# Kernel tuning notes

Measured on AMD Instinct MI355X. Metric: run time of the kernel, lower is better.

## Reference

```python
import jax, jax.numpy as jnp
import numpy as np

N = 12288
F_IN = 128
F_OUT = 128


def setup_inputs() -> dict:
    key = jax.random.key(0)
    k1, k2, k3, k4, k5, k6, k7 = jax.random.split(key, 7)
    stdv = 1.0 / np.sqrt(F_OUT)
    return {
        "feats": jax.random.normal(k1, (N, F_IN), dtype=jnp.float32),
        "node_adj": jax.random.normal(k2, (N, N), dtype=jnp.float32),
        "edge_adj": jax.random.normal(k3, (N, N), dtype=jnp.float32),
        # params: msg_type='concat' -> node_weight is [2*in, out]
        "node_weight": jax.random.uniform(k4, (2 * F_IN, F_OUT), dtype=jnp.float32, minval=-stdv, maxval=stdv),
        "node_bias": jax.random.uniform(k5, (F_OUT,), dtype=jnp.float32, minval=-stdv, maxval=stdv),
        "edge_weight": jax.random.uniform(k6, (F_IN, F_OUT), dtype=jnp.float32, minval=-stdv, maxval=stdv),
        "edge_bias": jax.random.uniform(k7, (F_OUT,), dtype=jnp.float32, minval=-stdv, maxval=stdv),
    }


def reference(feats, node_adj, edge_adj, node_weight, node_bias, edge_weight, edge_bias):
    # msg_type == 'concat': two masked spmms over signed adjacency, concat along features
    pos = (node_adj > 0).astype(feats.dtype)  # [N, N]
    neg = (node_adj < 0).astype(feats.dtype)  # [N, N]
    node_support = jnp.concatenate([pos @ feats, neg @ feats], axis=1)  # [N, 2*F_IN]
    node_output = node_support @ node_weight + node_bias  # [N, F_OUT]
    edge_support = edge_adj @ feats  # [N, F_IN]
    edge_output = edge_support @ edge_weight + edge_bias  # [N, F_OUT]
    return jax.nn.relu(node_output) + edge_output
```

## Files before the change

kernel.cpp:

```cpp
#include <hip/hip_runtime.h>
#include <stdint.h>

#define N_ROWS 12288
#define GSZ (128 * 12288)
#define NPART_OFF (9437184 / 4)
#define EPART_OFF ((9437184 + 6291456) / 4)

typedef __attribute__((ext_vector_type(8))) short bf16x8;
typedef __attribute__((ext_vector_type(4))) float f32x4;

__device__ __forceinline__ uint32_t f2bf(float x) {
  union { float f; uint32_t u; } c; c.f = x;
  return (c.u + 0x7FFFu + ((c.u >> 16) & 1u)) >> 16;
}
__device__ __forceinline__ uint32_t pk_bf(float a, float b) {
  return f2bf(a) | (f2bf(b) << 16);
}
__device__ __forceinline__ uint32_t pk_pos(float a, float b) {
  return (a > 0.f ? 0x3F80u : 0u) | (b > 0.f ? 0x3F800000u : 0u);
}
__device__ __forceinline__ uint32_t pk_neg(float a, float b) {
  return (a < 0.f ? 0x3F80u : 0u) | (b < 0.f ? 0x3F800000u : 0u);
}

__global__ __launch_bounds__(256) void gw_kernel(
    const float* __restrict__ feats, const float* __restrict__ node_w,
    const float* __restrict__ edge_w, uint16_t* __restrict__ gt) {
  __shared__ float lf[16 * 128];
  const int t = threadIdx.x;
  const int kb = blockIdx.x * 16;
  {
    const float4* src = (const float4*)(feats + (size_t)kb * 128);
    float4* dst = (float4*)lf;
    dst[t] = src[t];
    dst[t + 256] = src[t + 256];
  }
  __syncthreads();
  const int n = t & 127;
  const int rh = t >> 7;
  const float* wb[3] = {node_w, node_w + 128 * 128, edge_w};
#pragma unroll
  for (int j = 0; j < 3; ++j) {
    const float* W = wb[j] + n;
    float acc[8];
#pragma unroll
    for (int q = 0; q < 8; ++q) acc[q] = 0.f;
    for (int i = 0; i < 128; i += 4) {
      const float w0 = W[(i + 0) * 128];
      const float w1 = W[(i + 1) * 128];
      const float w2 = W[(i + 2) * 128];
      const float w3 = W[(i + 3) * 128];
#pragma unroll
      for (int q = 0; q < 8; ++q) {
        const float4 f = *(const float4*)&lf[(rh * 8 + q) * 128 + i];
        acc[q] = fmaf(f.w, w3, fmaf(f.z, w2, fmaf(f.y, w1, fmaf(f.x, w0, acc[q]))));
      }
    }
    uint4 o;
    o.x = pk_bf(acc[0], acc[1]);
    o.y = pk_bf(acc[2], acc[3]);
    o.z = pk_bf(acc[4], acc[5]);
    o.w = pk_bf(acc[6], acc[7]);
    *(uint4*)(gt + (size_t)j * GSZ + (size_t)n * N_ROWS + kb + rh * 8) = o;
  }
}

__global__ __launch_bounds__(256, 3) void fgc_main(
    const float* __restrict__ node_adj, const float* __restrict__ edge_adj,
    const uint16_t* __restrict__ gt, float* __restrict__ node_part,
    float* __restrict__ edge_part) {
  __shared__ __align__(128) char smem[49152];
  const int t = threadIdx.x;
  const int l = t & 63;
  const int w = t >> 6;
  const int bid = blockIdx.x;
  const int slice = (bid >> 1) & 3;
  const int rowt = ((bid >> 3) << 1) | (bid & 1);
  const int row0 = rowt * 64;
  const size_t k0 = (size_t)slice * 3072;

  const int r = t >> 2, q4 = t & 3;
  const float* np_ = node_adj + (size_t)(row0 + r) * N_ROWS + k0 + q4 * 16;
  const float* ep_ = edge_adj + (size_t)(row0 + r) * N_ROWS + k0 + q4 * 16;
  const int g0 = q4 * 2, g1 = q4 * 2 + 1;
  const int wOffA = r * 128 + ((g0 ^ (r & 7)) * 16);
  const int wOffB = r * 128 + ((g1 ^ (r & 7)) * 16);

  const int arow = (l & 15) * 128;
  const int rx = l & 7;
  const int gq = l >> 4;

  const uint16_t* gB = gt + (size_t)(w * 32 + (l & 15)) * N_ROWS + k0 + gq * 8;

  f32x4 accn[4][2], acce[4][2];
#pragma unroll
  for (int a = 0; a < 4; ++a)
#pragma unroll
    for (int b = 0; b < 2; ++b) {
      accn[a][b] = {0.f, 0.f, 0.f, 0.f};
      acce[a][b] = {0.f, 0.f, 0.f, 0.f};
    }

  float4 rn0, rn1, rn2, rn3, re0, re1, re2, re3;
  rn0 = *(const float4*)(np_);
  rn1 = *(const float4*)(np_ + 4);
  rn2 = *(const float4*)(np_ + 8);
  rn3 = *(const float4*)(np_ + 12);
  re0 = *(const float4*)(ep_);
  re1 = *(const float4*)(ep_ + 4);
  re2 = *(const float4*)(ep_ + 8);
  re3 = *(const float4*)(ep_ + 12);

  for (int kt = 0; kt < 48; ++kt) {
    char* wb2 = smem + (kt & 1) * 24576;
    {
      uint4 P;
      P.x = pk_pos(rn0.x, rn0.y); P.y = pk_pos(rn0.z, rn0.w);
      P.z = pk_pos(rn1.x, rn1.y); P.w = pk_pos(rn1.z, rn1.w);
      *(uint4*)(wb2 + wOffA) = P;
      P.x = pk_pos(rn2.x, rn2.y); P.y = pk_pos(rn2.z, rn2.w);
      P.z = pk_pos(rn3.x, rn3.y); P.w = pk_pos(rn3.z, rn3.w);
      *(uint4*)(wb2 + wOffB) = P;
      P.x = pk_neg(rn0.x, rn0.y); P.y = pk_neg(rn0.z, rn0.w);
      P.z = pk_neg(rn1.x, rn1.y); P.w = pk_neg(rn1.z, rn1.w);
      *(uint4*)(wb2 + 8192 + wOffA) = P;
      P.x = pk_neg(rn2.x, rn2.y); P.y = pk_neg(rn2.z, rn2.w);
      P.z = pk_neg(rn3.x, rn3.y); P.w = pk_neg(rn3.z, rn3.w);
      *(uint4*)(wb2 + 8192 + wOffB) = P;
      P.x = pk_bf(re0.x, re0.y);  P.y = pk_bf(re0.z, re0.w);
      P.z = pk_bf(re1.x, re1.y);  P.w = pk_bf(re1.z, re1.w);
      *(uint4*)(wb2 + 16384 + wOffA) = P;
      P.x = pk_bf(re2.x, re2.y);  P.y = pk_bf(re2.z, re2.w);
      P.z = pk_bf(re3.x, re3.y);  P.w = pk_bf(re3.z, re3.w);
      *(uint4*)(wb2 + 16384 + wOffB) = P;
    }
    __syncthreads();
    if (kt < 47) {
      const size_t ko = (size_t)(kt + 1) * 64;
      rn0 = *(const float4*)(np_ + ko);
      rn1 = *(const float4*)(np_ + ko + 4);
      rn2 = *(const float4*)(np_ + ko + 8);
      rn3 = *(const float4*)(np_ + ko + 12);
      re0 = *(const float4*)(ep_ + ko);
      re1 = *(const float4*)(ep_ + ko + 4);
      re2 = *(const float4*)(ep_ + ko + 8);
      re3 = *(const float4*)(ep_ + ko + 12);
    }
    const char* rb = smem + (kt & 1) * 24576;
#pragma unroll
    for (int ks = 0; ks < 2; ++ks) {
      const int a0 = arow + (((ks * 4 + gq) ^ rx) * 16);
      const uint16_t* gk = gB + kt * 64 + ks * 32;
      {
        bf16x8 ap[4], an[4];
#pragma unroll
        for (int mf = 0; mf < 4; ++mf) {
          ap[mf] = *(const bf16x8*)(rb + a0 + mf * 2048);
          an[mf] = *(const bf16x8*)(rb + 8192 + a0 + mf * 2048);
        }
#pragma unroll
        for (int nf = 0; nf < 2; ++nf) {
          const uint16_t* gp = gk + (size_t)nf * 16 * N_ROWS;
          const bf16x8 b1 = *(const bf16x8*)(gp);
          const bf16x8 b2 = *(const bf16x8*)(gp + GSZ);
#pragma unroll
          for (int mf = 0; mf < 4; ++mf)
            accn[mf][nf] = __builtin_amdgcn_mfma_f32_16x16x32_bf16(ap[mf], b1, accn[mf][nf], 0, 0, 0);
#pragma unroll
          for (int mf = 0; mf < 4; ++mf)
            accn[mf][nf] = __builtin_amdgcn_mfma_f32_16x16x32_bf16(an[mf], b2, accn[mf][nf], 0, 0, 0);
        }
      }
      {
        bf16x8 ae[4];
#pragma unroll
        for (int mf = 0; mf < 4; ++mf)
          ae[mf] = *(const bf16x8*)(rb + 16384 + a0 + mf * 2048);
#pragma unroll
        for (int nf = 0; nf < 2; ++nf) {
          const bf16x8 b3 = *(const bf16x8*)(gk + (size_t)nf * 16 * N_ROWS + 2 * GSZ);
#pragma unroll
          for (int mf = 0; mf < 4; ++mf)
            acce[mf][nf] = __builtin_amdgcn_mfma_f32_16x16x32_bf16(ae[mf], b3, acce[mf][nf], 0, 0, 0);
        }
      }
    }
  }

#pragma unroll
  for (int nf = 0; nf < 2; ++nf) {
    const int col = w * 32 + nf * 16 + (l & 15);
#pragma unroll
    for (int mf = 0; mf < 4; ++mf) {
      const f32x4 nv = accn[mf][nf];
      const f32x4 ev = acce[mf][nf];
#pragma unroll
      for (int q = 0; q < 4; ++q) {
        const size_t idx = (size_t)(row0 + mf * 16 + gq * 4 + q) * 128 + col;
        unsafeAtomicAdd(&node_part[idx], nv[q]);
        unsafeAtomicAdd(&edge_part[idx], ev[q]);
      }
    }
  }
}

__global__ __launch_bounds__(256) void fgc_final(
    const float* __restrict__ node_part, const float* __restrict__ edge_part,
    const float* __restrict__ node_bias, const float* __restrict__ edge_bias,
    float* __restrict__ out) {
  const int idx = blockIdx.x * 256 + threadIdx.x;
  const int col = (idx * 4) & 127;
  const float4 n = ((const float4*)node_part)[idx];
  const float4 e = ((const float4*)edge_part)[idx];
  const float4 nb = *(const float4*)(node_bias + col);
  const float4 eb = *(const float4*)(edge_bias + col);
  float4 o;
  o.x = fmaxf(n.x + nb.x, 0.f) + e.x + eb.x;
  o.y = fmaxf(n.y + nb.y, 0.f) + e.y + eb.y;
  o.z = fmaxf(n.z + nb.z, 0.f) + e.z + eb.z;
  o.w = fmaxf(n.w + nb.w, 0.f) + e.w + eb.w;
  ((float4*)out)[idx] = o;
}

extern "C" void kernel_launch(void* const* d_in, const int* in_sizes, int n_in,
                              void* d_out, int out_size, void* d_ws, size_t ws_size,
                              hipStream_t stream) {
  const float* feats = (const float*)d_in[0];
  const float* node_adj = (const float*)d_in[1];
  const float* edge_adj = (const float*)d_in[2];
  const float* node_w = (const float*)d_in[3];
  const float* node_b = (const float*)d_in[4];
  const float* edge_w = (const float*)d_in[5];
  const float* edge_b = (const float*)d_in[6];
  uint16_t* gt = (uint16_t*)d_ws;
  float* node_part = (float*)d_ws + NPART_OFF;
  float* edge_part = (float*)d_ws + EPART_OFF;

  gw_kernel<<<768, 256, 0, stream>>>(feats, node_w, edge_w, gt);
  hipMemsetAsync((char*)d_ws + 9437184, 0, 2 * 6291456, stream);
  fgc_main<<<768, 256, 0, stream>>>(node_adj, edge_adj, gt,
                                    node_part, edge_part);
  fgc_final<<<1536, 256, 0, stream>>>(node_part, edge_part, node_b, edge_b,
                                      (float*)d_out);
}
```

Before: 423.5 us.

## Prefetch B fragments before barrier and use nontemporal adjacency loads

Result: slower. 561.0 us (+32.5%).

```diff
diff --git a/kernel.cpp b/kernel.cpp
--- a/kernel.cpp
+++ b/kernel.cpp
@@ -8,6 +8,7 @@
 
 typedef __attribute__((ext_vector_type(8))) short bf16x8;
 typedef __attribute__((ext_vector_type(4))) float f32x4;
+typedef __attribute__((ext_vector_type(4))) float f32x4v;
 
 __device__ __forceinline__ uint32_t f2bf(float x) {
   union { float f; uint32_t u; } c; c.f = x;
@@ -65,7 +66,7 @@
   }
 }
 
-__global__ __launch_bounds__(256, 3) void fgc_main(
+__global__ __launch_bounds__(256) void fgc_main(
     const float* __restrict__ node_adj, const float* __restrict__ edge_adj,
     const uint16_t* __restrict__ gt, float* __restrict__ node_part,
     float* __restrict__ edge_part) {
@@ -101,17 +102,32 @@
       acce[a][b] = {0.f, 0.f, 0.f, 0.f};
     }
 
-  float4 rn0, rn1, rn2, rn3, re0, re1, re2, re3;
-  rn0 = *(const float4*)(np_);
-  rn1 = *(const float4*)(np_ + 4);
-  rn2 = *(const float4*)(np_ + 8);
-  rn3 = *(const float4*)(np_ + 12);
-  re0 = *(const float4*)(ep_);
-  re1 = *(const float4*)(ep_ + 4);
-  re2 = *(const float4*)(ep_ + 8);
-  re3 = *(const float4*)(ep_ + 12);
+  f32x4v rn0, rn1, rn2, rn3, re0, re1, re2, re3;
+  rn0 = __builtin_nontemporal_load((const f32x4v*)(np_));
+  rn1 = __builtin_nontemporal_load((const f32x4v*)(np_ + 4));
+  rn2 = __builtin_nontemporal_load((const f32x4v*)(np_ + 8));
+  rn3 = __builtin_nontemporal_load((const f32x4v*)(np_ + 12));
+  re0 = __builtin_nontemporal_load((const f32x4v*)(ep_));
+  re1 = __builtin_nontemporal_load((const f32x4v*)(ep_ + 4));
+  re2 = __builtin_nontemporal_load((const f32x4v*)(ep_ + 8));
+  re3 = __builtin_nontemporal_load((const f32x4v*)(ep_ + 12));
 
   for (int kt = 0; kt < 48; ++kt) {
+    bf16x8 Bv[2][2][3];
+    {
+      const uint16_t* gk = gB + kt * 64;
+#pragma unroll
+      for (int ks = 0; ks < 2; ++ks)
+#pragma unroll
+        for (int nf = 0; nf < 2; ++nf) {
+          const uint16_t* gp = gk + ks * 32 + (size_t)nf * 16 * N_ROWS;
+          Bv[ks][nf][0] = *(const bf16x8*)(gp);
+          Bv[ks][nf][1] = *(const bf16x8*)(gp + GSZ);
+          Bv[ks][nf][2] = *(const bf16x8*)(gp + 2 * GSZ);
+        }
+    }
+    __builtin_amdgcn_sched_barrier(0);
+
     char* wb2 = smem + (kt & 1) * 24576;
     {
       uint4 P;
@@ -134,55 +150,45 @@
       P.z = pk_bf(re3.x, re3.y);  P.w = pk_bf(re3.z, re3.w);
       *(uint4*)(wb2 + 16384 + wOffB) = P;
     }
-    __syncthreads();
+
     if (kt < 47) {
       const size_t ko = (size_t)(kt + 1) * 64;
-      rn0 = *(const float4*)(np_ + ko);
-      rn1 = *(const float4*)(np_ + ko + 4);
-      rn2 = *(const float4*)(np_ + ko + 8);
-      rn3 = *(const float4*)(np_ + ko + 12);
-      re0 = *(const float4*)(ep_ + ko);
-      re1 = *(const float4*)(ep_ + ko + 4);
-      re2 = *(const float4*)(ep_ + ko + 8);
-      re3 = *(const float4*)(ep_ + ko + 12);
-    }
+      rn0 = __builtin_nontemporal_load((const f32x4v*)(np_ + ko));
+      rn1 = __builtin_nontemporal_load((const f32x4v*)(np_ + ko + 4));
+      rn2 = __builtin_nontemporal_load((const f32x4v*)(np_ + ko + 8));
+      rn3 = __builtin_nontemporal_load((const f32x4v*)(np_ + ko + 12));
+      re0 = __builtin_nontemporal_load((const f32x4v*)(ep_ + ko));
+      re1 = __builtin_nontemporal_load((const f32x4v*)(ep_ + ko + 4));
+      re2 = __builtin_nontemporal_load((const f32x4v*)(ep_ + ko + 8));
+      re3 = __builtin_nontemporal_load((const f32x4v*)(ep_ + ko + 12));
+    }
+
+    asm volatile("s_waitcnt lgkmcnt(0)" ::: "memory");
+    __builtin_amdgcn_sched_barrier(0);
+    __builtin_amdgcn_s_barrier();
+
     const char* rb = smem + (kt & 1) * 24576;
 #pragma unroll
     for (int ks = 0; ks < 2; ++ks) {
       const int a0 = arow + (((ks * 4 + gq) ^ rx) * 16);
-      const uint16_t* gk = gB + kt * 64 + ks * 32;
-      {
-        bf16x8 ap[4], an[4];
-#pragma unroll
-        for (int mf = 0; mf < 4; ++mf) {
-          ap[mf] = *(const bf16x8*)(rb + a0 + mf * 2048);
-          an[mf] = *(const bf16x8*)(rb + 8192 + a0 + mf * 2048);
-        }
-#pragma unroll
-        for (int nf = 0; nf < 2; ++nf) {
-          const uint16_t* gp = gk + (size_t)nf * 16 * N_ROWS;
-          const bf16x8 b1 = *(const bf16x8*)(gp);
-          const bf16x8 b2 = *(const bf16x8*)(gp + GSZ);
-#pragma unroll
-          for (int mf = 0; mf < 4; ++mf)
-            accn[mf][nf] = __builtin_amdgcn_mfma_f32_16x16x32_bf16(ap[mf], b1, accn[mf][nf], 0, 0, 0);
-#pragma unroll
-          for (int mf = 0; mf < 4; ++mf)
-            accn[mf][nf] = __builtin_amdgcn_mfma_f32_16x16x32_bf16(an[mf], b2, accn[mf][nf], 0, 0, 0);
-        }
-      }
-      {
-        bf16x8 ae[4];
+      bf16x8 ap[4], an[4], ae[4];
+#pragma unroll
+      for (int mf = 0; mf < 4; ++mf) {
+        ap[mf] = *(const bf16x8*)(rb + a0 + mf * 2048);
+        an[mf] = *(const bf16x8*)(rb + 8192 + a0 + mf * 2048);
+        ae[mf] = *(const bf16x8*)(rb + 16384 + a0 + mf * 2048);
+      }
+#pragma unroll
+      for (int nf = 0; nf < 2; ++nf) {
 #pragma unroll
         for (int mf = 0; mf < 4; ++mf)
-          ae[mf] = *(const bf16x8*)(rb + 16384 + a0 + mf * 2048);
-#pragma unroll
-        for (int nf = 0; nf < 2; ++nf) {
-          const bf16x8 b3 = *(const bf16x8*)(gk + (size_t)nf * 16 * N_ROWS + 2 * GSZ);
-#pragma unroll
-          for (int mf = 0; mf < 4; ++mf)
-            acce[mf][nf] = __builtin_amdgcn_mfma_f32_16x16x32_bf16(ae[mf], b3, acce[mf][nf], 0, 0, 0);
-        }
+          accn[mf][nf] = __builtin_amdgcn_mfma_f32_16x16x32_bf16(ap[mf], Bv[ks][nf][0], accn[mf][nf], 0, 0, 0);
+#pragma unroll
+        for (int mf = 0; mf < 4; ++mf)
+          accn[mf][nf] = __builtin_amdgcn_mfma_f32_16x16x32_bf16(an[mf], Bv[ks][nf][1], accn[mf][nf], 0, 0, 0);
+#pragma unroll
+        for (int mf = 0; mf < 4; ++mf)
+          acce[mf][nf] = __builtin_amdgcn_mfma_f32_16x16x32_bf16(ae[mf], Bv[ks][nf][2], acce[mf][nf], 0, 0, 0);
       }
     }
   }
```
